# Performance work log

Hardware: AMD Instinct MI355X
Metric: run time of the kernel (lower is better)

## Reference

```python
import jax, jax.numpy as jnp
import numpy as np

NODES = 256
D0, D1 = 0.0, 1.0


def setup_inputs() -> dict:
    key = jax.random.key(0)
    k1, k2 = jax.random.split(key)
    inp = jax.random.uniform(k1, (32, 1024, 1024), dtype=jnp.float32)
    # learnable knot values, initialized as linspace over the domain (as in nn.Parameter)
    value = jnp.linspace(D0, D1, NODES, dtype=jnp.float32)
    # perturb so the spline is non-trivial (still a valid parameter state)
    value = value + 0.1 * jax.random.normal(k2, (NODES,), dtype=jnp.float32)
    return {"input": inp, "value": value}


def _akima_node_slopes(value, h):
    # interval slopes m_i = (v_{i+1}-v_i)/h, shape [n-1]
    m = (value[1:] - value[:-1]) / h
    # Akima boundary extension: two extra slopes on each side
    m_m1 = 2.0 * m[0] - m[1]
    m_m2 = 2.0 * m_m1 - m[0]
    m_p1 = 2.0 * m[-1] - m[-2]
    m_p2 = 2.0 * m_p1 - m[-1]
    me = jnp.concatenate([jnp.stack([m_m2, m_m1]), m, jnp.stack([m_p1, m_p2])])  # [n+3]
    # node derivative s_i = (|m_{i+1}-m_i|*m_{i-1} + |m_{i-1}-m_{i-2}|*m_i) / (sum)
    w1 = jnp.abs(me[3:] - me[2:-1])   # |m_{i+1} - m_i|,      [n]
    w2 = jnp.abs(me[1:-2] - me[:-3])  # |m_{i-1} - m_{i-2}|,  [n]
    mi_1 = me[1:-2]  # m_{i-1}
    mi = me[2:-1]    # m_i
    denom = w1 + w2
    safe = jnp.where(denom > 0, denom, 1.0)
    return jnp.where(denom > 0, (w1 * mi_1 + w2 * mi) / safe, 0.5 * (mi_1 + mi))


def reference(input, value):
    n = value.shape[0]
    h = (D1 - D0) / (n - 1)
    s = _akima_node_slopes(value, h)  # [n]
    x = jnp.clip(input, D0, D1)
    t = (x - D0) / h
    idx = jnp.clip(jnp.floor(t).astype(jnp.int32), 0, n - 2)
    u = t - idx.astype(x.dtype)  # local coordinate in [0,1]
    v0 = value[idx]
    v1 = value[idx + 1]
    s0 = s[idx]
    s1 = s[idx + 1]
    u2 = u * u
    u3 = u2 * u
    h00 = 2.0 * u3 - 3.0 * u2 + 1.0
    h10 = u3 - 2.0 * u2 + u
    h01 = -2.0 * u3 + 3.0 * u2
    h11 = u3 - u2
    return h00 * v0 + h10 * h * s0 + h01 * v1 + h11 * h * s1
```

## Files before the change

### kernel.cpp

```cpp
#include <hip/hip_runtime.h>
#include <hip/hip_bf16.h>

#define NODES 256

typedef float f32x4 __attribute__((ext_vector_type(4)));

__global__ __launch_bounds__(256) void akima_prologue(
    const float* __restrict__ value, float4* __restrict__ tab) {
  __shared__ float me[NODES + 3];
  __shared__ float s[NODES];
  const int t = threadIdx.x;
  const float h = 1.0f / 255.0f;

  if (t < NODES - 1) me[t + 2] = (value[t + 1] - value[t]) / h;
  __syncthreads();
  if (t == 0) {
    float m0 = me[2], m1 = me[3];
    float m_m1 = 2.0f * m0 - m1;
    me[1] = m_m1;
    me[0] = 2.0f * m_m1 - m0;
    float mL = me[NODES], mL1 = me[NODES - 1];
    float m_p1 = 2.0f * mL - mL1;
    me[NODES + 1] = m_p1;
    me[NODES + 2] = 2.0f * m_p1 - mL;
  }
  __syncthreads();
  {
    float w1 = fabsf(me[t + 3] - me[t + 2]);
    float w2 = fabsf(me[t + 1] - me[t]);
    float denom = w1 + w2;
    s[t] = (denom > 0.0f) ? (w1 * me[t + 1] + w2 * me[t + 2]) / denom
                          : 0.5f * (me[t + 1] + me[t + 2]);
  }
  __syncthreads();
  if (t < NODES - 1)
    tab[t] = make_float4(value[t], value[t + 1], s[t], s[t + 1]);
}

__device__ __forceinline__ float akima_eval(float x, const float4& c) {
  const float h = 1.0f / 255.0f;
  float tt = fminf(fmaxf(x, 0.0f), 1.0f) * 255.0f;
  int idx = min(max((int)tt, 0), NODES - 2);
  float u = tt - (float)idx;
  float u2 = u * u;
  float u3 = u2 * u;
  float h00 = 2.0f * u3 - 3.0f * u2 + 1.0f;
  float h10 = u3 - 2.0f * u2 + u;
  float h01 = -2.0f * u3 + 3.0f * u2;
  float h11 = u3 - u2;
  return h00 * c.x + h10 * h * c.z + h01 * c.y + h11 * h * c.w;
}

__device__ __forceinline__ int akima_idx(float x) {
  float tt = fminf(fmaxf(x, 0.0f), 1.0f) * 255.0f;
  return min(max((int)tt, 0), NODES - 2);
}

__global__ __launch_bounds__(256) void akima_main(
    const float* __restrict__ in, const float4* __restrict__ gtab,
    float* __restrict__ out, long long n, long long n4) {
  __shared__ float4 stab[NODES - 1];
  if (threadIdx.x < NODES - 1) stab[threadIdx.x] = gtab[threadIdx.x];
  __syncthreads();

  const f32x4* __restrict__ in4 = reinterpret_cast<const f32x4*>(in);
  f32x4* __restrict__ out4 = reinterpret_cast<f32x4*>(out);
  const long long stride = (long long)gridDim.x * blockDim.x;
  const long long i0 = (long long)blockIdx.x * blockDim.x + threadIdx.x;

  for (long long i = i0; i < n4; i += stride) {
    f32x4 x4 = __builtin_nontemporal_load(&in4[i]);

    int ia = akima_idx(x4.x);
    int ib = akima_idx(x4.y);
    int ic = akima_idx(x4.z);
    int id = akima_idx(x4.w);
    float4 ca = stab[ia];
    float4 cb = gtab[ib];
    float4 cc = stab[ic];
    float4 cd = gtab[id];

    f32x4 r;
    r.x = akima_eval(x4.x, ca);
    r.y = akima_eval(x4.y, cb);
    r.z = akima_eval(x4.z, cc);
    r.w = akima_eval(x4.w, cd);
    __builtin_nontemporal_store(r, &out4[i]);
  }

  for (long long i = n4 * 4 + i0; i < n; i += stride) {
    float x = in[i];
    float4 c = stab[akima_idx(x)];
    out[i] = akima_eval(x, c);
  }
}

extern "C" void kernel_launch(void* const* d_in, const int* in_sizes, int n_in,
                              void* d_out, int out_size, void* d_ws, size_t ws_size,
                              hipStream_t stream) {
  const float* in = (const float*)d_in[0];
  const float* value = (const float*)d_in[1];
  float* out = (float*)d_out;
  float4* tab = (float4*)d_ws;

  long long n = (long long)in_sizes[0];
  long long n4 = n / 4;

  akima_prologue<<<1, 256, 0, stream>>>(value, tab);

  long long want = (n4 + 255) / 256;
  int blocks = (int)(want < 2048 ? (want > 0 ? want : 1) : 2048);
  akima_main<<<blocks, 256, 0, stream>>>(in, tab, out, n, n4);
}
```

Before: 227.8 us.

## Precompute cubic polynomial coefficients and drop LDS table with one-element-per-thread grid

The prologue now stores per-interval power-basis cubic coefficients instead of the raw values and slopes, so each element needs a single Horner evaluation rather than computing the Hermite basis. The main kernel no longer stages the table in shared memory; all four lookups read the 4 KB table from global memory and rely on cache. The grid-stride loop is replaced by one float4 per thread with a grid sized to cover the whole array. This trims per-element ALU work and the per-block table copy and barrier, at the cost of more blocks and gathers that go through the cache instead of LDS.

```diff
diff --git a/kernel.cpp b/kernel.cpp
--- a/kernel.cpp
+++ b/kernel.cpp
@@ -6,7 +6,7 @@
 typedef float f32x4 __attribute__((ext_vector_type(4)));
 
 __global__ __launch_bounds__(256) void akima_prologue(
-    const float* __restrict__ value, float4* __restrict__ tab) {
+    const float* __restrict__ value, f32x4* __restrict__ tab) {
   __shared__ float me[NODES + 3];
   __shared__ float s[NODES];
   const int t = threadIdx.x;
@@ -33,65 +33,61 @@
                           : 0.5f * (me[t + 1] + me[t + 2]);
   }
   __syncthreads();
-  if (t < NODES - 1)
-    tab[t] = make_float4(value[t], value[t + 1], s[t], s[t + 1]);
+  if (t < NODES - 1) {
+    float v0 = value[t], v1 = value[t + 1];
+    float hs0 = h * s[t], hs1 = h * s[t + 1];
+    f32x4 c;
+    c.x = v0;
+    c.y = hs0;
+    c.z = 3.0f * (v1 - v0) - 2.0f * hs0 - hs1;
+    c.w = 2.0f * (v0 - v1) + hs0 + hs1;
+    tab[t] = c;
+  }
 }
 
-__device__ __forceinline__ float akima_eval(float x, const float4& c) {
-  const float h = 1.0f / 255.0f;
+__device__ __forceinline__ float akima_poly(float x, const f32x4& c) {
   float tt = fminf(fmaxf(x, 0.0f), 1.0f) * 255.0f;
-  int idx = min(max((int)tt, 0), NODES - 2);
+  int idx = min((int)tt, NODES - 2);
   float u = tt - (float)idx;
-  float u2 = u * u;
-  float u3 = u2 * u;
-  float h00 = 2.0f * u3 - 3.0f * u2 + 1.0f;
-  float h10 = u3 - 2.0f * u2 + u;
-  float h01 = -2.0f * u3 + 3.0f * u2;
-  float h11 = u3 - u2;
-  return h00 * c.x + h10 * h * c.z + h01 * c.y + h11 * h * c.w;
+  return c.x + u * (c.y + u * (c.z + u * c.w));
 }
 
 __device__ __forceinline__ int akima_idx(float x) {
   float tt = fminf(fmaxf(x, 0.0f), 1.0f) * 255.0f;
-  return min(max((int)tt, 0), NODES - 2);
+  return min((int)tt, NODES - 2);
 }
 
 __global__ __launch_bounds__(256) void akima_main(
-    const float* __restrict__ in, const float4* __restrict__ gtab,
+    const float* __restrict__ in, const f32x4* __restrict__ gtab,
     float* __restrict__ out, long long n, long long n4) {
-  __shared__ float4 stab[NODES - 1];
-  if (threadIdx.x < NODES - 1) stab[threadIdx.x] = gtab[threadIdx.x];
-  __syncthreads();
-
+  const long long i = (long long)blockIdx.x * blockDim.x + threadIdx.x;
   const f32x4* __restrict__ in4 = reinterpret_cast<const f32x4*>(in);
   f32x4* __restrict__ out4 = reinterpret_cast<f32x4*>(out);
-  const long long stride = (long long)gridDim.x * blockDim.x;
-  const long long i0 = (long long)blockIdx.x * blockDim.x + threadIdx.x;
 
-  for (long long i = i0; i < n4; i += stride) {
+  if (i < n4) {
     f32x4 x4 = __builtin_nontemporal_load(&in4[i]);
-
     int ia = akima_idx(x4.x);
     int ib = akima_idx(x4.y);
     int ic = akima_idx(x4.z);
     int id = akima_idx(x4.w);
-    float4 ca = stab[ia];
-    float4 cb = gtab[ib];
-    float4 cc = stab[ic];
-    float4 cd = gtab[id];
-
+    f32x4 ca = gtab[ia];
+    f32x4 cb = gtab[ib];
+    f32x4 cc = gtab[ic];
+    f32x4 cd = gtab[id];
     f32x4 r;
-    r.x = akima_eval(x4.x, ca);
-    r.y = akima_eval(x4.y, cb);
-    r.z = akima_eval(x4.z, cc);
-    r.w = akima_eval(x4.w, cd);
+    r.x = akima_poly(x4.x, ca);
+    r.y = akima_poly(x4.y, cb);
+    r.z = akima_poly(x4.z, cc);
+    r.w = akima_poly(x4.w, cd);
     __builtin_nontemporal_store(r, &out4[i]);
   }
 
-  for (long long i = n4 * 4 + i0; i < n; i += stride) {
-    float x = in[i];
-    float4 c = stab[akima_idx(x)];
-    out[i] = akima_eval(x, c);
+  if (blockIdx.x == 0) {
+    long long j = n4 * 4 + threadIdx.x;
+    if (j < n) {
+      float x = in[j];
+      out[j] = akima_poly(x, gtab[akima_idx(x)]);
+    }
   }
 }
 
@@ -101,14 +97,14 @@
   const float* in = (const float*)d_in[0];
   const float* value = (const float*)d_in[1];
   float* out = (float*)d_out;
-  float4* tab = (float4*)d_ws;
+  f32x4* tab = (f32x4*)d_ws;
 
   long long n = (long long)in_sizes[0];
   long long n4 = n / 4;
 
   akima_prologue<<<1, 256, 0, stream>>>(value, tab);
 
-  long long want = (n4 + 255) / 256;
-  int blocks = (int)(want < 2048 ? (want > 0 ? want : 1) : 2048);
-  akima_main<<<blocks, 256, 0, stream>>>(in, tab, out, n, n4);
+  long long blocks = (n4 + 255) / 256;
+  if (blocks < 1) blocks = 1;
+  akima_main<<<(int)blocks, 256, 0, stream>>>(in, tab, out, n, n4);
 }
```

Result: no change. 229.9 us (+0.9%).
